# Performance work log

Measured on AMD Instinct MI355X. Metric: run time of the kernel, lower is better.

The kernel has to match this reference:

```python
import jax, jax.numpy as jnp
import numpy as np

P = 2            # power (even positive int)
TEMPERATURE = 1.0
SCALE = 1.0 / np.sqrt(64.0)  # sqrt(head_dim) scaling
EPS = 1e-6


def setup_inputs() -> dict:
    key = jax.random.key(0)
    kq, kk, kv = jax.random.split(key, 3)
    shape = (4, 16, 2048, 64)  # (B, H, N, head_dim)
    return {
        "q": jax.random.normal(kq, shape, dtype=jnp.float32),
        "k": jax.random.normal(kk, shape, dtype=jnp.float32),
        "v": jax.random.normal(kv, shape, dtype=jnp.float32),
    }


def reference(q, k, v):
    # logits = q @ k^T * scale / temperature : (B, H, N, N)
    logits = jnp.einsum("bhnd,bhmd->bhnm", q, k) * (SCALE / TEMPERATURE)
    attn = logits ** P
    attn = attn / (attn.sum(axis=-1, keepdims=True) + EPS)
    return jnp.einsum("bhnm,bhmd->bhnd", attn, v)
```

## Files before the change

### kernel.cpp

```cpp
#include <hip/hip_runtime.h>

#define N_CTX 2048
#define DHEAD 64
#define SCALE_F 0.125f
#define EPS_F 1e-6f
#define KT 64
#define NITER (N_CTX / KT)
#define QBLK 256

typedef __attribute__((ext_vector_type(8))) short short8;
typedef __attribute__((ext_vector_type(4))) float float4v;
typedef __attribute__((ext_vector_type(2))) unsigned uint2v;
typedef __attribute__((ext_vector_type(4))) unsigned uint4v;

#if defined(__HIP_DEVICE_COMPILE__) && __has_builtin(__builtin_amdgcn_cvt_pk_bf16_f32)
typedef __attribute__((ext_vector_type(2))) __bf16 bf16x2;
__device__ __forceinline__ unsigned pack2(float a, float b) {
    union { bf16x2 v; unsigned u; } x;
    x.v = __builtin_amdgcn_cvt_pk_bf16_f32(a, b);
    return x.u;
}
#else
__device__ __forceinline__ unsigned bf1(float f) {
    union { float f; unsigned u; } x; x.f = f;
    return (x.u + 0x7FFFu + ((x.u >> 16) & 1u)) >> 16;
}
__device__ __forceinline__ unsigned pack2(float a, float b) {
    return bf1(a) | (bf1(b) << 16);
}
#endif

#if defined(__HIP_DEVICE_COMPILE__) && __has_builtin(__builtin_amdgcn_permlane32_swap)
__device__ __forceinline__ void pl32(unsigned &x, unsigned &y) {
    uint2v r = __builtin_amdgcn_permlane32_swap(x, y, false, false);
    x = r[0]; y = r[1];
}
#else
__device__ __forceinline__ void pl32(unsigned &x, unsigned &y) {
    asm volatile("v_permlane32_swap_b32 %0, %1" : "+v"(x), "+v"(y));
}
#endif
#if defined(__HIP_DEVICE_COMPILE__) && __has_builtin(__builtin_amdgcn_permlane16_swap)
__device__ __forceinline__ void pl16(unsigned &x, unsigned &y) {
    uint2v r = __builtin_amdgcn_permlane16_swap(x, y, false, false);
    x = r[0]; y = r[1];
}
#else
__device__ __forceinline__ void pl16(unsigned &x, unsigned &y) {
    asm volatile("v_permlane16_swap_b32 %0, %1" : "+v"(x), "+v"(y));
}
#endif

__device__ __forceinline__ int swz(int row, int col) {
    return col ^ ((row & 7) << 3);
}


__global__ __launch_bounds__(256, 2)
void powsm_attn(const float* __restrict__ qg, const float* __restrict__ kg,
                const float* __restrict__ vg, float* __restrict__ og)
{
    __shared__ __align__(16) short KsB[2][64][64];
    __shared__ __align__(16) short VtB[2][64][64];
    __shared__ float Dn[4][64];

    const int bh   = blockIdx.y;
    const int tid  = threadIdx.x;
    const int wave = tid >> 6;
    const int lane = tid & 63;
    const int qd   = lane >> 4;
    const int c    = lane & 15;

    const size_t base = (size_t)bh * N_CTX * DHEAD;
    const float* qp = qg + base;
    const float* kp = kg + base;
    const float* vp = vg + base;
    float*       op = og + base;

    const int qw0 = blockIdx.x * QBLK + wave * 64;

    union { uint4v u; short8 s; } dvu;
    {
        const unsigned ob = (c == 0) ? 0x3F803F80u : 0u;
        dvu.u[0] = ob; dvu.u[1] = ob; dvu.u[2] = ob; dvu.u[3] = ob;
    }
    const short8 bfden = dvu.s;

    short8 Qf[4][2];
    #pragma unroll
    for (int qt = 0; qt < 4; ++qt) {
        #pragma unroll
        for (int ks = 0; ks < 2; ++ks) {
            const float* src = qp + (size_t)(qw0 + qt*16 + c) * DHEAD + ks*32 + qd*8;
            float4v a = *(const float4v*)(src);
            float4v b = *(const float4v*)(src + 4);
            uint4v u;
            u[0] = pack2(a[0]*SCALE_F, a[1]*SCALE_F);
            u[1] = pack2(a[2]*SCALE_F, a[3]*SCALE_F);
            u[2] = pack2(b[0]*SCALE_F, b[1]*SCALE_F);
            u[3] = pack2(b[2]*SCALE_F, b[3]*SCALE_F);
            union { uint4v u; short8 s; } cv; cv.u = u;
            Qf[qt][ks] = cv.s;
        }
    }

    float4v Oacc[4][4];
    #pragma unroll
    for (int qt = 0; qt < 4; ++qt)
        #pragma unroll
        for (int nt = 0; nt < 4; ++nt)
            Oacc[qt][nt] = (float4v){0.f, 0.f, 0.f, 0.f};
    float4v Oden[4];
    #pragma unroll
    for (int qt = 0; qt < 4; ++qt) Oden[qt] = (float4v){0.f, 0.f, 0.f, 0.f};

    const int kr = tid >> 4;
    const int kc = tid & 15;

    float4v pK[4], pV[4];
    #pragma unroll
    for (int u = 0; u < 4; ++u)
        pK[u] = *(const float4v*)(kp + (size_t)(kr + u*16) * DHEAD + kc*4);
    #pragma unroll
    for (int j = 0; j < 4; ++j)
        pV[j] = *(const float4v*)(vp + (size_t)(4*kr + j) * DHEAD + kc*4);

    {
        short (*Ks)[64] = KsB[0];
        short (*Vt)[64] = VtB[0];
        #pragma unroll
        for (int u = 0; u < 4; ++u) {
            const int row = kr + u*16;
            uint2v w; w[0] = pack2(pK[u][0], pK[u][1]); w[1] = pack2(pK[u][2], pK[u][3]);
            *(uint2v*)&Ks[row][swz(row, kc*4)] = w;
        }
        #pragma unroll
        for (int kk = 0; kk < 4; ++kk) {
            const int row = 4*kc + kk;
            uint2v w; w[0] = pack2(pV[0][kk], pV[1][kk]); w[1] = pack2(pV[2][kk], pV[3][kk]);
            *(uint2v*)&Vt[row][swz(row, 4*kr)] = w;
        }
    }
    __syncthreads();

    #pragma unroll 1
    for (int kvi = 0; kvi < NITER; ++kvi) {
        const int cur = kvi & 1;
        short (*Ks)[64] = KsB[cur];
        short (*Vt)[64] = VtB[cur];

        if (kvi + 1 < NITER) {
            const float* kn = kp + (size_t)(kvi + 1) * KT * DHEAD;
            const float* vn = vp + (size_t)(kvi + 1) * KT * DHEAD;
            #pragma unroll
            for (int u = 0; u < 4; ++u)
                pK[u] = *(const float4v*)(kn + (size_t)(kr + u*16) * DHEAD + kc*4);
            #pragma unroll
            for (int j = 0; j < 4; ++j)
                pV[j] = *(const float4v*)(vn + (size_t)(4*kr + j) * DHEAD + kc*4);
        }

        #pragma unroll
        for (int blk = 0; blk < 2; ++blk) {
            float4v slo[4], shi[4];
            #pragma unroll
            for (int qt = 0; qt < 4; ++qt) {
                slo[qt] = (float4v){0.f, 0.f, 0.f, 0.f};
                shi[qt] = (float4v){0.f, 0.f, 0.f, 0.f};
            }
            #pragma unroll
            for (int ks = 0; ks < 2; ++ks) {
                short8 afl = *(const short8*)&Ks[blk*32 + c][swz(c, ks*32 + qd*8)];
                #pragma unroll
                for (int qt = 0; qt < 4; ++qt)
                    slo[qt] = __builtin_amdgcn_mfma_f32_16x16x32_bf16(afl, Qf[qt][ks], slo[qt], 0, 0, 0);
            }
            #pragma unroll
            for (int ks = 0; ks < 2; ++ks) {
                short8 afh = *(const short8*)&Ks[blk*32 + 16 + c][swz(c, ks*32 + qd*8)];
                #pragma unroll
                for (int qt = 0; qt < 4; ++qt)
                    shi[qt] = __builtin_amdgcn_mfma_f32_16x16x32_bf16(afh, Qf[qt][ks], shi[qt], 0, 0, 0);
            }
            short8 pa[4];
            #pragma unroll
            for (int qt = 0; qt < 4; ++qt) {
                float4v psl = slo[qt] * slo[qt];
                float4v psh = shi[qt] * shi[qt];
                unsigned w00 = pack2(psl[0], psl[1]);
                unsigned w01 = pack2(psl[2], psl[3]);
                unsigned w10 = pack2(psh[0], psh[1]);
                unsigned w11 = pack2(psh[2], psh[3]);
                pl32(w00, w10);
                pl32(w01, w11);
                pl16(w00, w10);
                pl16(w01, w11);
                union { uint4v u; short8 s; } cv;
                cv.u[0] = w00; cv.u[1] = w01; cv.u[2] = w10; cv.u[3] = w11;
                pa[qt] = cv.s;
            }
            #pragma unroll
            for (int qt = 0; qt < 4; ++qt)
                Oden[qt] = __builtin_amdgcn_mfma_f32_16x16x32_bf16(pa[qt], bfden, Oden[qt], 0, 0, 0);
            #pragma unroll
            for (int nt = 0; nt < 4; ++nt) {
                short8 bf = *(const short8*)&Vt[nt*16 + c][swz(c, blk*32 + qd*8)];
                #pragma unroll
                for (int qt = 0; qt < 4; ++qt)
                    Oacc[qt][nt] = __builtin_amdgcn_mfma_f32_16x16x32_bf16(pa[qt], bf, Oacc[qt][nt], 0, 0, 0);
            }
        }

        if (kvi + 1 < NITER) {
            short (*Kn)[64] = KsB[cur ^ 1];
            short (*Vn)[64] = VtB[cur ^ 1];
            #pragma unroll
            for (int u = 0; u < 4; ++u) {
                const int row = kr + u*16;
                uint2v w; w[0] = pack2(pK[u][0], pK[u][1]); w[1] = pack2(pK[u][2], pK[u][3]);
                *(uint2v*)&Kn[row][swz(row, kc*4)] = w;
            }
            #pragma unroll
            for (int kk = 0; kk < 4; ++kk) {
                const int row = 4*kc + kk;
                uint2v w; w[0] = pack2(pV[0][kk], pV[1][kk]); w[1] = pack2(pV[2][kk], pV[3][kk]);
                *(uint2v*)&Vn[row][swz(row, 4*kr)] = w;
            }
        }
        __syncthreads();
    }

    if (c == 0) {
        #pragma unroll
        for (int qt = 0; qt < 4; ++qt)
            #pragma unroll
            for (int r = 0; r < 4; ++r)
                Dn[wave][qt*16 + qd*4 + r] = Oden[qt][r];
    }
    __syncthreads();

    #pragma unroll
    for (int qt = 0; qt < 4; ++qt) {
        #pragma unroll
        for (int r = 0; r < 4; ++r) {
            float inv = 1.0f / (Dn[wave][qt*16 + qd*4 + r] + EPS_F);
            float* dst = op + (size_t)(qw0 + qt*16 + qd*4 + r) * DHEAD + c;
            #pragma unroll
            for (int nt = 0; nt < 4; ++nt)
                dst[nt*16] = Oacc[qt][nt][r] * inv;
        }
    }
}

extern "C" void kernel_launch(void* const* d_in, const int* in_sizes, int n_in,
                              void* d_out, int out_size, void* d_ws, size_t ws_size,
                              hipStream_t stream) {
    const float* q = (const float*)d_in[0];
    const float* k = (const float*)d_in[1];
    const float* v = (const float*)d_in[2];
    float* out = (float*)d_out;
    dim3 grid(N_CTX / QBLK, 64, 1);
    powsm_attn<<<grid, dim3(256, 1, 1), 0, stream>>>(q, k, v, out);
}
```

Measured before the change: 200.6 us.

## Split KV sequence across two wave groups per block with shared-memory reduction

After: 761.4 us. 3.8x slower.

```diff
diff --git a/kernel.cpp b/kernel.cpp
--- a/kernel.cpp
+++ b/kernel.cpp
@@ -5,7 +5,7 @@
 #define SCALE_F 0.125f
 #define EPS_F 1e-6f
 #define KT 64
-#define NITER (N_CTX / KT)
+#define NSTEP (N_CTX / (2 * KT))
 #define QBLK 256
 
 typedef __attribute__((ext_vector_type(8))) short short8;
@@ -56,13 +56,13 @@
 }
 
 
-__global__ __launch_bounds__(256, 2)
+__global__ __launch_bounds__(512, 4)
 void powsm_attn(const float* __restrict__ qg, const float* __restrict__ kg,
                 const float* __restrict__ vg, float* __restrict__ og)
 {
     __shared__ __align__(16) short KsB[2][64][64];
     __shared__ __align__(16) short VtB[2][64][64];
-    __shared__ float Dn[4][64];
+    __shared__ float Dn[8][64];
 
     const int bh   = blockIdx.y;
     const int tid  = threadIdx.x;
@@ -70,6 +70,8 @@
     const int lane = tid & 63;
     const int qd   = lane >> 4;
     const int c    = lane & 15;
+    const int qgrp = wave & 3;
+    const int half = wave >> 2;
 
     const size_t base = (size_t)bh * N_CTX * DHEAD;
     const float* qp = qg + base;
@@ -77,7 +79,7 @@
     const float* vp = vg + base;
     float*       op = og + base;
 
-    const int qw0 = blockIdx.x * QBLK + wave * 64;
+    const int qw0 = blockIdx.x * QBLK + qgrp * 64;
 
     union { uint4v u; short8 s; } dvu;
     {
@@ -114,20 +116,23 @@
     #pragma unroll
     for (int qt = 0; qt < 4; ++qt) Oden[qt] = (float4v){0.f, 0.f, 0.f, 0.f};
 
-    const int kr = tid >> 4;
-    const int kc = tid & 15;
+    const int g  = tid >> 8;
+    const int st = tid & 255;
+    const int kr = st >> 4;
+    const int kc = st & 15;
 
     float4v pK[4], pV[4];
-    #pragma unroll
-    for (int u = 0; u < 4; ++u)
-        pK[u] = *(const float4v*)(kp + (size_t)(kr + u*16) * DHEAD + kc*4);
-    #pragma unroll
-    for (int j = 0; j < 4; ++j)
-        pV[j] = *(const float4v*)(vp + (size_t)(4*kr + j) * DHEAD + kc*4);
-
     {
-        short (*Ks)[64] = KsB[0];
-        short (*Vt)[64] = VtB[0];
+        const float* k0 = kp + (size_t)g * KT * DHEAD;
+        const float* v0 = vp + (size_t)g * KT * DHEAD;
+        #pragma unroll
+        for (int u = 0; u < 4; ++u)
+            pK[u] = *(const float4v*)(k0 + (size_t)(kr + u*16) * DHEAD + kc*4);
+        #pragma unroll
+        for (int j = 0; j < 4; ++j)
+            pV[j] = *(const float4v*)(v0 + (size_t)(4*kr + j) * DHEAD + kc*4);
+        short (*Ks)[64] = KsB[g];
+        short (*Vt)[64] = VtB[g];
         #pragma unroll
         for (int u = 0; u < 4; ++u) {
             const int row = kr + u*16;
@@ -144,14 +149,10 @@
     __syncthreads();
 
     #pragma unroll 1
-    for (int kvi = 0; kvi < NITER; ++kvi) {
-        const int cur = kvi & 1;
-        short (*Ks)[64] = KsB[cur];
-        short (*Vt)[64] = VtB[cur];
-
-        if (kvi + 1 < NITER) {
-            const float* kn = kp + (size_t)(kvi + 1) * KT * DHEAD;
-            const float* vn = vp + (size_t)(kvi + 1) * KT * DHEAD;
+    for (int t = 0; t < NSTEP; ++t) {
+        if (t + 1 < NSTEP) {
+            const float* kn = kp + (size_t)(2*(t+1) + g) * KT * DHEAD;
+            const float* vn = vp + (size_t)(2*(t+1) + g) * KT * DHEAD;
             #pragma unroll
             for (int u = 0; u < 4; ++u)
                 pK[u] = *(const float4v*)(kn + (size_t)(kr + u*16) * DHEAD + kc*4);
@@ -160,6 +161,8 @@
                 pV[j] = *(const float4v*)(vn + (size_t)(4*kr + j) * DHEAD + kc*4);
         }
 
+        short (*Ks)[64] = KsB[half];
+        short (*Vt)[64] = VtB[half];
         #pragma unroll
         for (int blk = 0; blk < 2; ++blk) {
             float4v slo[4], shi[4];
@@ -210,10 +213,11 @@
                     Oacc[qt][nt] = __builtin_amdgcn_mfma_f32_16x16x32_bf16(pa[qt], bf, Oacc[qt][nt], 0, 0, 0);
             }
         }
-
-        if (kvi + 1 < NITER) {
-            short (*Kn)[64] = KsB[cur ^ 1];
-            short (*Vn)[64] = VtB[cur ^ 1];
+        __syncthreads();
+
+        if (t + 1 < NSTEP) {
+            short (*Kn)[64] = KsB[g];
+            short (*Vn)[64] = VtB[g];
             #pragma unroll
             for (int u = 0; u < 4; ++u) {
                 const int row = kr + u*16;
@@ -239,15 +243,47 @@
     }
     __syncthreads();
 
-    #pragma unroll
-    for (int qt = 0; qt < 4; ++qt) {
-        #pragma unroll
-        for (int r = 0; r < 4; ++r) {
-            float inv = 1.0f / (Dn[wave][qt*16 + qd*4 + r] + EPS_F);
-            float* dst = op + (size_t)(qw0 + qt*16 + qd*4 + r) * DHEAD + c;
-            #pragma unroll
-            for (int nt = 0; nt < 4; ++nt)
-                dst[nt*16] = Oacc[qt][nt][r] * inv;
+    float* red0 = (float*)&KsB[0][0][0];
+    float* red1 = (float*)&VtB[0][0][0];
+    #pragma unroll 1
+    for (int rnd = 0; rnd < 2; ++rnd) {
+        if (half == 1 && (qgrp >> 1) == rnd) {
+            float* buf = (qgrp & 1) ? red1 : red0;
+            #pragma unroll
+            for (int qt = 0; qt < 4; ++qt)
+                #pragma unroll
+                for (int nt = 0; nt < 4; ++nt)
+                    #pragma unroll
+                    for (int r = 0; r < 4; ++r)
+                        buf[(qt*16 + qd*4 + r)*64 + nt*16 + c] = Oacc[qt][nt][r];
+        }
+        __syncthreads();
+        if (half == 0 && (qgrp >> 1) == rnd) {
+            float* buf = (qgrp & 1) ? red1 : red0;
+            #pragma unroll
+            for (int qt = 0; qt < 4; ++qt)
+                #pragma unroll
+                for (int nt = 0; nt < 4; ++nt)
+                    #pragma unroll
+                    for (int r = 0; r < 4; ++r)
+                        Oacc[qt][nt][r] += buf[(qt*16 + qd*4 + r)*64 + nt*16 + c];
+        }
+        __syncthreads();
+    }
+
+    if (half == 0) {
+        #pragma unroll
+        for (int qt = 0; qt < 4; ++qt) {
+            #pragma unroll
+            for (int r = 0; r < 4; ++r) {
+                const int idx = qt*16 + qd*4 + r;
+                float dsum = Dn[qgrp][idx] + Dn[4 + qgrp][idx];
+                float inv = 1.0f / (dsum + EPS_F);
+                float* dst = op + (size_t)(qw0 + idx) * DHEAD + c;
+                #pragma unroll
+                for (int nt = 0; nt < 4; ++nt)
+                    dst[nt*16] = Oacc[qt][nt][r] * inv;
+            }
         }
     }
 }
@@ -260,5 +296,5 @@
     const float* v = (const float*)d_in[2];
     float* out = (float*)d_out;
     dim3 grid(N_CTX / QBLK, 64, 1);
-    powsm_attn<<<grid, dim3(256, 1, 1), 0, stream>>>(q, k, v, out);
-}
+    powsm_attn<<<grid, dim3(512, 1, 1), 0, stream>>>(q, k, v, out);
+}
```
